# Optimization experiments

Hardware: AMD Instinct MI355X
Metric: run time of the kernel (lower is better)

## Reference

```python
import math
import jax, jax.numpy as jnp
import numpy as np

B, H, Nt, Nl, E = 4, 16, 512, 512, 64
P = H * E  # 1024, pre-projection embedding dim


def setup_inputs() -> dict:
    key = jax.random.key(0)
    ks = jax.random.split(key, 8)
    return {
        "projected_u": jax.random.normal(ks[0], (B, H, Nt, P), jnp.float32),
        "projected_b": jax.random.normal(ks[1], (B, H, Nt, 1), jnp.float32),
        "mu": jax.random.normal(ks[2], (B, Nl, P), jnp.float32),
        "logvar": jax.random.normal(ks[3], (B, Nl, P), jnp.float32) * 0.5,
        "pi": jax.random.uniform(ks[4], (B, Nl, 1), jnp.float32, 1e-3, 1.0),
        "w_v": jax.random.normal(ks[5], (H, E, P), jnp.float32) * 0.02,
        "b_v": jax.random.normal(ks[6], (H, E, Nl), jnp.float32) * 0.02,
        "attn_mask": jnp.zeros((B * H, 1, Nl), dtype=bool),  # True = masked
    }


def reference(projected_u, projected_b, mu, logvar, pi, w_v, b_v, attn_mask):
    Bq, Hq, Ntq, Pq = projected_u.shape
    Nlq = mu.shape[1]
    Eq = w_v.shape[1]
    prior_var_u = math.sqrt(Eq)

    var = jnp.exp(logvar)                         # [B,Nl,P]
    biased_var = var + prior_var_u                # [B,Nl,P]

    # float additive mask [B*H,1,Nl]: -inf where attn_mask True or pi<=0
    pi_rep = jnp.repeat(pi, Hq, axis=0)           # [B*H,Nl,1]
    am = jnp.where(attn_mask, -jnp.inf, 0.0)
    am = am + jnp.where(pi_rep.transpose(0, 2, 1) <= 0, -jnp.inf, 0.0)
    masked = jnp.isneginf(am).transpose(0, 2, 1)  # [B*H,Nl,1]

    # scores [B,H,Nt,Nl]
    attn = jnp.einsum('bhmp,bnp->bhmn', projected_u, mu / biased_var) + projected_b

    pi_c = jnp.maximum(pi_rep, jnp.finfo(pi_rep.dtype).tiny)
    t1 = jnp.where(masked, 0.0, jnp.log(pi_c))                                  # [B*H,Nl,1]
    t2 = 0.5 * jnp.sum((mu / jnp.sqrt(biased_var)) ** 2, axis=-1, keepdims=True)  # [B,Nl,1]
    t2 = jnp.repeat(t2, Hq, axis=0)                                             # [B*H,Nl,1]
    t3 = jnp.where(masked, 0.0, jnp.log(jnp.repeat(biased_var, Hq, axis=0)))    # [B*H,Nl,P]
    t3 = jnp.sum(0.5 * t3, axis=-1, keepdims=True)                              # [B*H,Nl,1]

    attn = attn + (t1 - t2 - t3).reshape(Bq, Hq, Nlq, 1).transpose(0, 1, 3, 2)  # [B,H,1,Nl]
    attn = attn + am.reshape(Bq, Hq, 1, Nlq)
    attn = jax.nn.softmax(attn, axis=-1)                                        # [B,H,Nt,Nl]

    # denoised values: interpolation between query projection and means
    out = (jnp.einsum('bhmn,bnp->bhmp', attn, var / biased_var) * projected_u
           + jnp.einsum('bhmn,bnp->bhmp', attn, (prior_var_u / biased_var) * mu))  # [B,H,Nt,P]
    out = (jnp.einsum('bhmp,hep->bhme', out, w_v)
           + jnp.einsum('bhmn,hen->bhme', attn, b_v))                              # [B,H,Nt,E]
    return (out.reshape(Bq * Hq, Ntq, Eq), attn.reshape(Bq * Hq, Ntq, Nlq))
```

## Files before the change

### kernel.cpp

```cpp
#include <hip/hip_runtime.h>
#include <cstdint>
#include <cstddef>
#include <cmath>

#define B_  4
#define H_  16
#define NT  512
#define NL  512
#define E_  64
#define P_  1024
#define HE  1024
#define BH  64

typedef __attribute__((ext_vector_type(8))) short short8;
typedef __attribute__((ext_vector_type(4))) float f32x4;
typedef unsigned short u16;

#define MFMA(a, b, c) __builtin_amdgcn_mfma_f32_16x16x32_bf16(a, b, c, 0, 0, 0)

static __device__ inline u16 f2bf_rne(float f) {
  unsigned u = __float_as_uint(f);
  unsigned r = u + 0x7FFFu + ((u >> 16) & 1u);
  return (u16)(r >> 16);
}

static __device__ inline void gl_lds16(const void* g, void* l) {
  __builtin_amdgcn_global_load_lds(
      (const __attribute__((address_space(1))) void*)g,
      (__attribute__((address_space(3))) void*)l, 16, 0, 0);
}

__global__ __launch_bounds__(256) void k_precompute(
    const float* __restrict__ mu, const float* __restrict__ logvar,
    const float* __restrict__ pi, u16* __restrict__ mobv_hi,
    u16* __restrict__ mobv_lo, u16* __restrict__ ibvT,
    float* __restrict__ bias) {
  const int bn = blockIdx.x;
  const int b = bn >> 9, n = bn & 511;
  const int t = threadIdx.x;
  const size_t base = (size_t)bn * P_;
  float t2 = 0.f, t3 = 0.f;
#pragma unroll
  for (int i = 0; i < P_ / 256; ++i) {
    const int p = t + i * 256;
    const float lv  = logvar[base + p];
    const float v   = expf(lv);
    const float bv  = v + 8.0f;
    const float inv = 1.0f / bv;
    const float m   = mu[base + p];
    const float x   = m * inv;
    const unsigned bits = __float_as_uint(x);
    mobv_hi[base + p] = (u16)(bits >> 16);
    const float r = x - __uint_as_float(bits & 0xFFFF0000u);
    mobv_lo[base + p] = (u16)(__float_as_uint(r) >> 16);
    ibvT[((size_t)b * P_ + p) * NL + n] = f2bf_rne(inv);
    t2 += m * x;
    t3 += logf(bv);
  }
  __shared__ float r2[256];
  __shared__ float r3[256];
  r2[t] = t2; r3[t] = t3;
  __syncthreads();
  for (int s = 128; s > 0; s >>= 1) {
    if (t < s) { r2[t] += r2[t + s]; r3[t] += r3[t + s]; }
    __syncthreads();
  }
  if (t == 0) {
    const float pv = pi[bn];
    float bb;
    if (pv <= 0.f) bb = -INFINITY;
    else bb = logf(fmaxf(pv, 1.17549435e-38f)) - 0.5f * r2[0] - 0.5f * r3[0];
    bias[bn] = bb;
  }
}

__global__ __launch_bounds__(256) void k_wvcast(const float* __restrict__ wv,
                                                u16* __restrict__ wvb) {
  const int i = (blockIdx.x * 256 + threadIdx.x) * 4;
  const float4 f = *(const float4*)&wv[i];
  wvb[i + 0] = f2bf_rne(f.x);
  wvb[i + 1] = f2bf_rne(f.y);
  wvb[i + 2] = f2bf_rne(f.z);
  wvb[i + 3] = f2bf_rne(f.w);
}

__global__ __launch_bounds__(256) void k_w2p(
    const u16* __restrict__ mobv_hi, const u16* __restrict__ mobv_lo,
    const u16* __restrict__ wvb, const float* __restrict__ bv_,
    u16* __restrict__ W2pT) {
  const int b    = blockIdx.z;
  const int row0 = blockIdx.x * 64;
  const int col0 = blockIdx.y * 128;
  const int t = threadIdx.x;
  const int wave = t >> 6, lane = t & 63;
  const int l16 = lane & 15, sel = lane >> 4;
  const int mrow = (wave >> 1) * 32, ncol = (wave & 1) * 64;

  __shared__ u16 Ah[64 * 32];
  __shared__ u16 Al[64 * 32];
  __shared__ u16 Bs[128 * 32];

  const u16* Abh = mobv_hi + ((size_t)b * NL + row0) * P_;
  const u16* Abl = mobv_lo + ((size_t)b * NL + row0) * P_;
  const u16* Bb  = wvb + (size_t)col0 * P_;

  f32x4 acc[2][4];
#pragma unroll
  for (int i = 0; i < 2; ++i)
#pragma unroll
    for (int j = 0; j < 4; ++j) acc[i][j] = (f32x4){0.f, 0.f, 0.f, 0.f};

  for (int k0 = 0; k0 < P_; k0 += 32) {
    {
      const int c = t;
      const int row = c >> 2, k8 = (c & 3) ^ ((row >> 1) & 3);
      gl_lds16(Abh + (size_t)row * P_ + k0 + k8 * 8, &Ah[wave * 64 * 8]);
      gl_lds16(Abl + (size_t)row * P_ + k0 + k8 * 8, &Al[wave * 64 * 8]);
    }
#pragma unroll
    for (int i = 0; i < 2; ++i) {
      const int c = t + i * 256;
      const int row = c >> 2, k8 = (c & 3) ^ ((row >> 1) & 3);
      gl_lds16(Bb + (size_t)row * P_ + k0 + k8 * 8,
               &Bs[(i * 256 + wave * 64) * 8]);
    }
    __syncthreads();
    short8 ah[2], al[2], bf[4];
#pragma unroll
    for (int mt = 0; mt < 2; ++mt) {
      const int r = mrow + mt * 16 + l16;
      const int ch = sel ^ ((r >> 1) & 3);
      ah[mt] = *(const short8*)&Ah[r * 32 + ch * 8];
      al[mt] = *(const short8*)&Al[r * 32 + ch * 8];
    }
#pragma unroll
    for (int nt = 0; nt < 4; ++nt) {
      const int r = ncol + nt * 16 + l16;
      const int ch = sel ^ ((r >> 1) & 3);
      bf[nt] = *(const short8*)&Bs[r * 32 + ch * 8];
    }
#pragma unroll
    for (int mt = 0; mt < 2; ++mt)
#pragma unroll
      for (int nt = 0; nt < 4; ++nt) {
        acc[mt][nt] = MFMA(ah[mt], bf[nt], acc[mt][nt]);
        acc[mt][nt] = MFMA(al[mt], bf[nt], acc[mt][nt]);
      }
    __syncthreads();
  }
#pragma unroll
  for (int mt = 0; mt < 2; ++mt) {
    const int nbase = row0 + mrow + mt * 16 + sel * 4;
#pragma unroll
    for (int nt = 0; nt < 4; ++nt) {
      const int he = col0 + ncol + nt * 16 + l16;
      const float4 bvv = *(const float4*)&bv_[(size_t)he * NL + nbase];
      ushort4 o;
      o.x = f2bf_rne(8.0f * acc[mt][nt][0] + bvv.x);
      o.y = f2bf_rne(8.0f * acc[mt][nt][1] + bvv.y);
      o.z = f2bf_rne(8.0f * acc[mt][nt][2] + bvv.z);
      o.w = f2bf_rne(8.0f * acc[mt][nt][3] + bvv.w);
      *(ushort4*)&W2pT[((size_t)b * HE + he) * NL + nbase] = o;
    }
  }
}

__global__ __launch_bounds__(256) void k_scores(
    const float* __restrict__ U, const u16* __restrict__ mobv_hi,
    const u16* __restrict__ mobv_lo, const float* __restrict__ pb,
    const float* __restrict__ bias, const uint8_t* __restrict__ mask,
    float* __restrict__ attn) {
  const int b    = blockIdx.z;
  const int row0 = blockIdx.x * 128;
  const int col0 = blockIdx.y * 128;
  const int t = threadIdx.x;
  const int wave = t >> 6, lane = t & 63;
  const int l16 = lane & 15, sel = lane >> 4;
  const int mrow = (wave >> 1) * 64, ncol = (wave & 1) * 64;

  __shared__ u16 Ah[128 * 32];
  __shared__ u16 Al[128 * 32];
  __shared__ u16 Bh[128 * 32];
  __shared__ u16 Bl[128 * 32];

  const u16* Bbh = mobv_hi + ((size_t)b * NL + col0) * P_;
  const u16* Bbl = mobv_lo + ((size_t)b * NL + col0) * P_;

  const int arow = t >> 1;
  const int ak   = (t & 1) * 16;
  const float* Aptr = U + ((size_t)b * 8192 + row0 + arow) * P_ + ak;
  const int asw = (arow >> 1) & 3;
  const int ch0 = ((t & 1) * 2 + 0) ^ asw;
  const int ch1 = ((t & 1) * 2 + 1) ^ asw;
  u16* AhW0 = &Ah[arow * 32 + ch0 * 8];
  u16* AhW1 = &Ah[arow * 32 + ch1 * 8];
  u16* AlW0 = &Al[arow * 32 + ch0 * 8];
  u16* AlW1 = &Al[arow * 32 + ch1 * 8];

  f32x4 acc[4][4];
#pragma unroll
  for (int i = 0; i < 4; ++i)
#pragma unroll
    for (int j = 0; j < 4; ++j) acc[i][j] = (f32x4){0.f, 0.f, 0.f, 0.f};

  for (int k0 = 0; k0 < P_; k0 += 32) {
    const float4 a0 = *(const float4*)&Aptr[k0 + 0];
    const float4 a1 = *(const float4*)&Aptr[k0 + 4];
    const float4 a2 = *(const float4*)&Aptr[k0 + 8];
    const float4 a3 = *(const float4*)&Aptr[k0 + 12];
#pragma unroll
    for (int i = 0; i < 2; ++i) {
      const int c = t + i * 256;
      const int row = c >> 2, k8 = (c & 3) ^ ((row >> 1) & 3);
      gl_lds16(Bbh + (size_t)row * P_ + k0 + k8 * 8,
               &Bh[(i * 256 + wave * 64) * 8]);
      gl_lds16(Bbl + (size_t)row * P_ + k0 + k8 * 8,
               &Bl[(i * 256 + wave * 64) * 8]);
    }
    const float av[16] = {a0.x, a0.y, a0.z, a0.w, a1.x, a1.y, a1.z, a1.w,
                          a2.x, a2.y, a2.z, a2.w, a3.x, a3.y, a3.z, a3.w};
    short8 h0, h1, l0, l1;
#pragma unroll
    for (int j = 0; j < 8; ++j) {
      unsigned bits = __float_as_uint(av[j]);
      h0[j] = (short)(bits >> 16);
      float rr = av[j] - __uint_as_float(bits & 0xFFFF0000u);
      l0[j] = (short)(__float_as_uint(rr) >> 16);
      bits = __float_as_uint(av[8 + j]);
      h1[j] = (short)(bits >> 16);
      rr = av[8 + j] - __uint_as_float(bits & 0xFFFF0000u);
      l1[j] = (short)(__float_as_uint(rr) >> 16);
    }
    *(short8*)AhW0 = h0;
    *(short8*)AhW1 = h1;
    *(short8*)AlW0 = l0;
    *(short8*)AlW1 = l1;
    __syncthreads();

    short8 ah[4], al[4], bh[4], bl[4];
#pragma unroll
    for (int mt = 0; mt < 4; ++mt) {
      const int r = mrow + mt * 16 + l16;
      const int ch = sel ^ ((r >> 1) & 3);
      ah[mt] = *(const short8*)&Ah[r * 32 + ch * 8];
      al[mt] = *(const short8*)&Al[r * 32 + ch * 8];
    }
#pragma unroll
    for (int nt = 0; nt < 4; ++nt) {
      const int r = ncol + nt * 16 + l16;
      const int ch = sel ^ ((r >> 1) & 3);
      bh[nt] = *(const short8*)&Bh[r * 32 + ch * 8];
      bl[nt] = *(const short8*)&Bl[r * 32 + ch * 8];
    }
#pragma unroll
    for (int mt = 0; mt < 4; ++mt)
#pragma unroll
      for (int nt = 0; nt < 4; ++nt) {
        acc[mt][nt] = MFMA(ah[mt], bh[nt], acc[mt][nt]);
        acc[mt][nt] = MFMA(ah[mt], bl[nt], acc[mt][nt]);
        acc[mt][nt] = MFMA(al[mt], bh[nt], acc[mt][nt]);
      }
    __syncthreads();
  }

  const int bh_ = b * H_ + (row0 >> 9);
  float pbv[4][4];
#pragma unroll
  for (int mt = 0; mt < 4; ++mt)
#pragma unroll
    for (int r = 0; r < 4; ++r)
      pbv[mt][r] = pb[(size_t)b * 8192 + row0 + mrow + mt * 16 + sel * 4 + r];
#pragma unroll
  for (int nt = 0; nt < 4; ++nt) {
    const int n = col0 + ncol + nt * 16 + l16;
    const float bcol = bias[b * NL + n];
    const bool mk = mask[(size_t)bh_ * NL + n] != 0;
#pragma unroll
    for (int mt = 0; mt < 4; ++mt) {
#pragma unroll
      for (int r = 0; r < 4; ++r) {
        const int row = row0 + mrow + mt * 16 + sel * 4 + r;
        float s = acc[mt][nt][r] + pbv[mt][r] + bcol;
        if (mk) s = -INFINITY;
        attn[((size_t)b * 8192 + row) * NL + n] = s;
      }
    }
  }
}

__global__ __launch_bounds__(256) void k_softmax(float* __restrict__ attn,
                                                 u16* __restrict__ attn_bf) {
  const int t = threadIdx.x;
  const int wave = t >> 6, lane = t & 63;
  const size_t r = (size_t)blockIdx.x * 4 + wave;
  float* row = attn + r * NL;
  const float4 v0 = ((const float4*)row)[lane * 2];
  const float4 v1 = ((const float4*)row)[lane * 2 + 1];
  float m = fmaxf(fmaxf(fmaxf(v0.x, v0.y), fmaxf(v0.z, v0.w)),
                  fmaxf(fmaxf(v1.x, v1.y), fmaxf(v1.z, v1.w)));
#pragma unroll
  for (int off = 32; off > 0; off >>= 1) m = fmaxf(m, __shfl_xor(m, off, 64));
  float e[8];
  e[0] = expf(v0.x - m); e[1] = expf(v0.y - m);
  e[2] = expf(v0.z - m); e[3] = expf(v0.w - m);
  e[4] = expf(v1.x - m); e[5] = expf(v1.y - m);
  e[6] = expf(v1.z - m); e[7] = expf(v1.w - m);
  float s = ((e[0] + e[1]) + (e[2] + e[3])) + ((e[4] + e[5]) + (e[6] + e[7]));
#pragma unroll
  for (int off = 32; off > 0; off >>= 1) s += __shfl_xor(s, off, 64);
  const float inv = 1.0f / s;
  float4 o0, o1;
  o0.x = e[0] * inv; o0.y = e[1] * inv; o0.z = e[2] * inv; o0.w = e[3] * inv;
  o1.x = e[4] * inv; o1.y = e[5] * inv; o1.z = e[6] * inv; o1.w = e[7] * inv;
  ((float4*)row)[lane * 2] = o0;
  ((float4*)row)[lane * 2 + 1] = o1;
  ushort4 b0, b1;
  b0.x = f2bf_rne(o0.x); b0.y = f2bf_rne(o0.y);
  b0.z = f2bf_rne(o0.z); b0.w = f2bf_rne(o0.w);
  b1.x = f2bf_rne(o1.x); b1.y = f2bf_rne(o1.y);
  b1.z = f2bf_rne(o1.z); b1.w = f2bf_rne(o1.w);
  ((ushort4*)(attn_bf + r * NL))[lane * 2] = b0;
  ((ushort4*)(attn_bf + r * NL))[lane * 2 + 1] = b1;
}

__global__ __launch_bounds__(256) void k_mid(
    const u16* __restrict__ attn_bf, const u16* __restrict__ ibvT,
    const float* __restrict__ U, u16* __restrict__ opS) {
  const int b    = blockIdx.z;
  const int row0 = blockIdx.x * 128;
  const int col0 = blockIdx.y * 128;
  const int t = threadIdx.x;
  const int wave = t >> 6, lane = t & 63;
  const int l16 = lane & 15, sel = lane >> 4;
  const int mrow = (wave >> 1) * 64, ncol = (wave & 1) * 64;

  __shared__ u16 As[128 * 32];
  __shared__ u16 Bs[128 * 32];

  const u16* Ab = attn_bf + ((size_t)b * 8192 + row0) * NL;
  const u16* Bb = ibvT + ((size_t)b * P_ + col0) * NL;

  f32x4 acc[4][4];
#pragma unroll
  for (int i = 0; i < 4; ++i)
#pragma unroll
    for (int j = 0; j < 4; ++j) acc[i][j] = (f32x4){0.f, 0.f, 0.f, 0.f};

  for (int k0 = 0; k0 < NL; k0 += 32) {
#pragma unroll
    for (int i = 0; i < 2; ++i) {
      const int c = t + i * 256;
      const int row = c >> 2, k8 = (c & 3) ^ ((row >> 1) & 3);
      gl_lds16(Ab + (size_t)row * NL + k0 + k8 * 8,
               &As[(i * 256 + wave * 64) * 8]);
      gl_lds16(Bb + (size_t)row * NL + k0 + k8 * 8,
               &Bs[(i * 256 + wave * 64) * 8]);
    }
    __syncthreads();
    short8 af[4], bf[4];
#pragma unroll
    for (int mt = 0; mt < 4; ++mt) {
      const int r = mrow + mt * 16 + l16;
      const int ch = sel ^ ((r >> 1) & 3);
      af[mt] = *(const short8*)&As[r * 32 + ch * 8];
    }
#pragma unroll
    for (int nt = 0; nt < 4; ++nt) {
      const int r = ncol + nt * 16 + l16;
      const int ch = sel ^ ((r >> 1) & 3);
      bf[nt] = *(const short8*)&Bs[r * 32 + ch * 8];
    }
#pragma unroll
    for (int mt = 0; mt < 4; ++mt)
#pragma unroll
      for (int nt = 0; nt < 4; ++nt)
        acc[mt][nt] = MFMA(af[mt], bf[nt], acc[mt][nt]);
    __syncthreads();
  }

#pragma unroll
  for (int mt = 0; mt < 4; ++mt) {
#pragma unroll
    for (int r = 0; r < 4; ++r) {
      const int m = row0 + mrow + mt * 16 + sel * 4 + r;
      const float* Urow = U + ((size_t)b * 8192 + m) * P_;
      u16* orow = opS + ((size_t)b * 8192 + m) * P_;
#pragma unroll
      for (int nt = 0; nt < 4; ++nt) {
        const int p = col0 + ncol + nt * 16 + l16;
        const float u = Urow[p];
        orow[p] = f2bf_rne((1.0f - 8.0f * acc[mt][nt][r]) * u);
      }
    }
  }
}

__global__ __launch_bounds__(256) void k_out2(
    const u16* __restrict__ opS, const u16* __restrict__ attn_bf,
    const u16* __restrict__ wvb, const u16* __restrict__ W2pT,
    float* __restrict__ out) {
  const int bh = blockIdx.y;
  const int b = bh >> 4, h = bh & 15;
  const int row0g = bh * NT + blockIdx.x * 64;
  const int t = threadIdx.x;
  const int wave = t >> 6, lane = t & 63;
  const int l16 = lane & 15, sel = lane >> 4;
  const int mrow = (wave >> 1) * 32, ncol = (wave & 1) * 32;

  __shared__ u16 As[64 * 64];
  __shared__ u16 Bs[64 * 64];

  f32x4 acc[2][2];
#pragma unroll
  for (int i = 0; i < 2; ++i)
#pragma unroll
    for (int j = 0; j < 2; ++j) acc[i][j] = (f32x4){0.f, 0.f, 0.f, 0.f};

  const u16* Ab1 = opS + (size_t)row0g * P_;
  const u16* Bb1 = wvb + (size_t)(h * 64) * P_;
  for (int k0 = 0; k0 < P_; k0 += 64) {
#pragma unroll
    for (int i = 0; i < 2; ++i) {
      const int c = t + i * 256;
      const int row = c >> 3, k8 = (c & 7) ^ (row & 7);
      gl_lds16(Ab1 + (size_t)row * P_ + k0 + k8 * 8,
               &As[(i * 256 + wave * 64) * 8]);
      gl_lds16(Bb1 + (size_t)row * P_ + k0 + k8 * 8,
               &Bs[(i * 256 + wave * 64) * 8]);
    }
    __syncthreads();
    short8 af[2][2], bf[2][2];
#pragma unroll
    for (int mt = 0; mt < 2; ++mt) {
      const int r = mrow + mt * 16 + l16;
#pragma unroll
      for (int kk = 0; kk < 2; ++kk) {
        const int ch = (kk * 4 + sel) ^ (r & 7);
        af[mt][kk] = *(const short8*)&As[r * 64 + ch * 8];
      }
    }
#pragma unroll
    for (int nt = 0; nt < 2; ++nt) {
      const int r = ncol + nt * 16 + l16;
#pragma unroll
      for (int kk = 0; kk < 2; ++kk) {
        const int ch = (kk * 4 + sel) ^ (r & 7);
        bf[nt][kk] = *(const short8*)&Bs[r * 64 + ch * 8];
      }
    }
#pragma unroll
    for (int mt = 0; mt < 2; ++mt)
#pragma unroll
      for (int nt = 0; nt < 2; ++nt) {
        acc[mt][nt] = MFMA(af[mt][0], bf[nt][0], acc[mt][nt]);
        acc[mt][nt] = MFMA(af[mt][1], bf[nt][1], acc[mt][nt]);
      }
    __syncthreads();
  }

  const u16* Ab2 = attn_bf + (size_t)row0g * NL;
  const u16* Bb2 = W2pT + ((size_t)b * HE + h * 64) * NL;
  for (int k0 = 0; k0 < NL; k0 += 64) {
#pragma unroll
    for (int i = 0; i < 2; ++i) {
      const int c = t + i * 256;
      const int row = c >> 3, k8 = (c & 7) ^ (row & 7);
      gl_lds16(Ab2 + (size_t)row * NL + k0 + k8 * 8,
               &As[(i * 256 + wave * 64) * 8]);
      gl_lds16(Bb2 + (size_t)row * NL + k0 + k8 * 8,
               &Bs[(i * 256 + wave * 64) * 8]);
    }
    __syncthreads();
    short8 af[2][2], bf[2][2];
#pragma unroll
    for (int mt = 0; mt < 2; ++mt) {
      const int r = mrow + mt * 16 + l16;
#pragma unroll
      for (int kk = 0; kk < 2; ++kk) {
        const int ch = (kk * 4 + sel) ^ (r & 7);
        af[mt][kk] = *(const short8*)&As[r * 64 + ch * 8];
      }
    }
#pragma unroll
    for (int nt = 0; nt < 2; ++nt) {
      const int r = ncol + nt * 16 + l16;
#pragma unroll
      for (int kk = 0; kk < 2; ++kk) {
        const int ch = (kk * 4 + sel) ^ (r & 7);
        bf[nt][kk] = *(const short8*)&Bs[r * 64 + ch * 8];
      }
    }
#pragma unroll
    for (int mt = 0; mt < 2; ++mt)
#pragma unroll
      for (int nt = 0; nt < 2; ++nt) {
        acc[mt][nt] = MFMA(af[mt][0], bf[nt][0], acc[mt][nt]);
        acc[mt][nt] = MFMA(af[mt][1], bf[nt][1], acc[mt][nt]);
      }
    __syncthreads();
  }

#pragma unroll
  for (int mt = 0; mt < 2; ++mt)
#pragma unroll
    for (int nt = 0; nt < 2; ++nt)
#pragma unroll
      for (int r = 0; r < 4; ++r) {
        const int row = row0g + mrow + mt * 16 + sel * 4 + r;
        const int e = ncol + nt * 16 + l16;
        out[(size_t)row * E_ + e] = acc[mt][nt][r];
      }
}

extern "C" void kernel_launch(void* const* d_in, const int* in_sizes, int n_in,
                              void* d_out, int out_size, void* d_ws, size_t ws_size,
                              hipStream_t stream) {
  const float*   u    = (const float*)d_in[0];
  const float*   pb   = (const float*)d_in[1];
  const float*   mu   = (const float*)d_in[2];
  const float*   logv = (const float*)d_in[3];
  const float*   pi   = (const float*)d_in[4];
  const float*   wv   = (const float*)d_in[5];
  const float*   bv   = (const float*)d_in[6];
  const uint8_t* mask = (const uint8_t*)d_in[7];

  float* out  = (float*)d_out;
  float* attn = out + (size_t)BH * NT * E_;

  u16*   mobv_hi = (u16*)d_ws;
  u16*   mobv_lo = mobv_hi + (size_t)B_ * NL * P_;
  u16*   ibvT    = mobv_lo + (size_t)B_ * NL * P_;
  u16*   W2pT    = ibvT + (size_t)B_ * P_ * NL;
  u16*   wvb     = W2pT + (size_t)B_ * HE * NL;
  float* bias    = (float*)(wvb + (size_t)HE * P_);
  u16*   attn_bf = (u16*)(bias + (size_t)B_ * NL);
  u16*   opS     = attn_bf + (size_t)BH * NT * NL;

  k_precompute<<<B_ * NL, 256, 0, stream>>>(mu, logv, pi, mobv_hi, mobv_lo,
                                            ibvT, bias);
  k_wvcast<<<(HE * P_) / 1024, 256, 0, stream>>>(wv, wvb);
  k_w2p<<<dim3(NL / 64, HE / 128, B_), 256, 0, stream>>>(mobv_hi, mobv_lo, wvb,
                                                         bv, W2pT);
  k_scores<<<dim3(8192 / 128, NL / 128, B_), 256, 0, stream>>>(
      u, mobv_hi, mobv_lo, pb, bias, mask, attn);
  k_softmax<<<(B_ * H_ * NT) / 4, 256, 0, stream>>>(attn, attn_bf);
  k_mid<<<dim3(8192 / 128, P_ / 128, B_), 256, 0, stream>>>(attn_bf, ibvT, u,
                                                            opS);
  k_out2<<<dim3(NT / 64, BH), 256, 0, stream>>>(opS, attn_bf, wvb, W2pT, out);
}
```

Measured before the change: 489.1 us.

## Double-buffer LDS tiles in score and mid GEMMs, stage fp32 A via direct loads

```diff
diff --git a/kernel.cpp b/kernel.cpp
--- a/kernel.cpp
+++ b/kernel.cpp
@@ -178,24 +178,13 @@
   const int l16 = lane & 15, sel = lane >> 4;
   const int mrow = (wave >> 1) * 64, ncol = (wave & 1) * 64;
 
-  __shared__ u16 Ah[128 * 32];
-  __shared__ u16 Al[128 * 32];
-  __shared__ u16 Bh[128 * 32];
-  __shared__ u16 Bl[128 * 32];
-
-  const u16* Bbh = mobv_hi + ((size_t)b * NL + col0) * P_;
-  const u16* Bbl = mobv_lo + ((size_t)b * NL + col0) * P_;
-
-  const int arow = t >> 1;
-  const int ak   = (t & 1) * 16;
-  const float* Aptr = U + ((size_t)b * 8192 + row0 + arow) * P_ + ak;
-  const int asw = (arow >> 1) & 3;
-  const int ch0 = ((t & 1) * 2 + 0) ^ asw;
-  const int ch1 = ((t & 1) * 2 + 1) ^ asw;
-  u16* AhW0 = &Ah[arow * 32 + ch0 * 8];
-  u16* AhW1 = &Ah[arow * 32 + ch1 * 8];
-  u16* AlW0 = &Al[arow * 32 + ch0 * 8];
-  u16* AlW1 = &Al[arow * 32 + ch1 * 8];
+  __shared__ float Af[2][128 * 32];
+  __shared__ u16   Bh[2][128 * 32];
+  __shared__ u16   Bl[2][128 * 32];
+
+  const float* Ab  = U + ((size_t)b * 8192 + row0) * P_;
+  const u16*   Bbh = mobv_hi + ((size_t)b * NL + col0) * P_;
+  const u16*   Bbl = mobv_lo + ((size_t)b * NL + col0) * P_;
 
   f32x4 acc[4][4];
 #pragma unroll
@@ -203,54 +192,54 @@
 #pragma unroll
     for (int j = 0; j < 4; ++j) acc[i][j] = (f32x4){0.f, 0.f, 0.f, 0.f};
 
-  for (int k0 = 0; k0 < P_; k0 += 32) {
-    const float4 a0 = *(const float4*)&Aptr[k0 + 0];
-    const float4 a1 = *(const float4*)&Aptr[k0 + 4];
-    const float4 a2 = *(const float4*)&Aptr[k0 + 8];
-    const float4 a3 = *(const float4*)&Aptr[k0 + 12];
+  auto stage = [&](int buf, int k0) {
+#pragma unroll
+    for (int i = 0; i < 4; ++i) {
+      const int c = t + i * 256;
+      const int row = c >> 3, k4 = (c & 7) ^ (row & 7);
+      gl_lds16(Ab + (size_t)row * P_ + k0 + k4 * 4,
+               &Af[buf][(i * 256 + wave * 64) * 4]);
+    }
 #pragma unroll
     for (int i = 0; i < 2; ++i) {
       const int c = t + i * 256;
       const int row = c >> 2, k8 = (c & 3) ^ ((row >> 1) & 3);
       gl_lds16(Bbh + (size_t)row * P_ + k0 + k8 * 8,
-               &Bh[(i * 256 + wave * 64) * 8]);
+               &Bh[buf][(i * 256 + wave * 64) * 8]);
       gl_lds16(Bbl + (size_t)row * P_ + k0 + k8 * 8,
-               &Bl[(i * 256 + wave * 64) * 8]);
-    }
-    const float av[16] = {a0.x, a0.y, a0.z, a0.w, a1.x, a1.y, a1.z, a1.w,
-                          a2.x, a2.y, a2.z, a2.w, a3.x, a3.y, a3.z, a3.w};
-    short8 h0, h1, l0, l1;
-#pragma unroll
-    for (int j = 0; j < 8; ++j) {
-      unsigned bits = __float_as_uint(av[j]);
-      h0[j] = (short)(bits >> 16);
-      float rr = av[j] - __uint_as_float(bits & 0xFFFF0000u);
-      l0[j] = (short)(__float_as_uint(rr) >> 16);
-      bits = __float_as_uint(av[8 + j]);
-      h1[j] = (short)(bits >> 16);
-      rr = av[8 + j] - __uint_as_float(bits & 0xFFFF0000u);
-      l1[j] = (short)(__float_as_uint(rr) >> 16);
-    }
-    *(short8*)AhW0 = h0;
-    *(short8*)AhW1 = h1;
-    *(short8*)AlW0 = l0;
-    *(short8*)AlW1 = l1;
-    __syncthreads();
+               &Bl[buf][(i * 256 + wave * 64) * 8]);
+    }
+  };
+
+  stage(0, 0);
+  __syncthreads();
+  int cur = 0;
+  for (int k0 = 0; k0 < P_; k0 += 32) {
+    if (k0 + 32 < P_) stage(cur ^ 1, k0 + 32);
 
     short8 ah[4], al[4], bh[4], bl[4];
 #pragma unroll
     for (int mt = 0; mt < 4; ++mt) {
       const int r = mrow + mt * 16 + l16;
-      const int ch = sel ^ ((r >> 1) & 3);
-      ah[mt] = *(const short8*)&Ah[r * 32 + ch * 8];
-      al[mt] = *(const short8*)&Al[r * 32 + ch * 8];
+      const int c0 = (sel * 2) ^ (r & 7);
+      const int c1 = (sel * 2 + 1) ^ (r & 7);
+      const float4 f0 = *(const float4*)&Af[cur][r * 32 + c0 * 4];
+      const float4 f1 = *(const float4*)&Af[cur][r * 32 + c1 * 4];
+      const float fv[8] = {f0.x, f0.y, f0.z, f0.w, f1.x, f1.y, f1.z, f1.w};
+#pragma unroll
+      for (int j = 0; j < 8; ++j) {
+        const unsigned bits = __float_as_uint(fv[j]);
+        ah[mt][j] = (short)(bits >> 16);
+        const float rr = fv[j] - __uint_as_float(bits & 0xFFFF0000u);
+        al[mt][j] = (short)(__float_as_uint(rr) >> 16);
+      }
     }
 #pragma unroll
     for (int nt = 0; nt < 4; ++nt) {
       const int r = ncol + nt * 16 + l16;
       const int ch = sel ^ ((r >> 1) & 3);
-      bh[nt] = *(const short8*)&Bh[r * 32 + ch * 8];
-      bl[nt] = *(const short8*)&Bl[r * 32 + ch * 8];
+      bh[nt] = *(const short8*)&Bh[cur][r * 32 + ch * 8];
+      bl[nt] = *(const short8*)&Bl[cur][r * 32 + ch * 8];
     }
 #pragma unroll
     for (int mt = 0; mt < 4; ++mt)
@@ -261,6 +250,7 @@
         acc[mt][nt] = MFMA(al[mt], bh[nt], acc[mt][nt]);
       }
     __syncthreads();
+    cur ^= 1;
   }
 
   const int bh_ = b * H_ + (row0 >> 9);
@@ -334,8 +324,8 @@
   const int l16 = lane & 15, sel = lane >> 4;
   const int mrow = (wave >> 1) * 64, ncol = (wave & 1) * 64;
 
-  __shared__ u16 As[128 * 32];
-  __shared__ u16 Bs[128 * 32];
+  __shared__ u16 As[2][128 * 32];
+  __shared__ u16 Bs[2][128 * 32];
 
   const u16* Ab = attn_bf + ((size_t)b * 8192 + row0) * NL;
   const u16* Bb = ibvT + ((size_t)b * P_ + col0) * NL;
@@ -346,29 +336,35 @@
 #pragma unroll
     for (int j = 0; j < 4; ++j) acc[i][j] = (f32x4){0.f, 0.f, 0.f, 0.f};
 
-  for (int k0 = 0; k0 < NL; k0 += 32) {
+  auto stage = [&](int buf, int k0) {
 #pragma unroll
     for (int i = 0; i < 2; ++i) {
       const int c = t + i * 256;
       const int row = c >> 2, k8 = (c & 3) ^ ((row >> 1) & 3);
       gl_lds16(Ab + (size_t)row * NL + k0 + k8 * 8,
-               &As[(i * 256 + wave * 64) * 8]);
+               &As[buf][(i * 256 + wave * 64) * 8]);
       gl_lds16(Bb + (size_t)row * NL + k0 + k8 * 8,
-               &Bs[(i * 256 + wave * 64) * 8]);
-    }
-    __syncthreads();
+               &Bs[buf][(i * 256 + wave * 64) * 8]);
+    }
+  };
+
+  stage(0, 0);
+  __syncthreads();
+  int cur = 0;
+  for (int k0 = 0; k0 < NL; k0 += 32) {
+    if (k0 + 32 < NL) stage(cur ^ 1, k0 + 32);
     short8 af[4], bf[4];
 #pragma unroll
     for (int mt = 0; mt < 4; ++mt) {
       const int r = mrow + mt * 16 + l16;
       const int ch = sel ^ ((r >> 1) & 3);
-      af[mt] = *(const short8*)&As[r * 32 + ch * 8];
+      af[mt] = *(const short8*)&As[cur][r * 32 + ch * 8];
     }
 #pragma unroll
     for (int nt = 0; nt < 4; ++nt) {
       const int r = ncol + nt * 16 + l16;
       const int ch = sel ^ ((r >> 1) & 3);
-      bf[nt] = *(const short8*)&Bs[r * 32 + ch * 8];
+      bf[nt] = *(const short8*)&Bs[cur][r * 32 + ch * 8];
     }
 #pragma unroll
     for (int mt = 0; mt < 4; ++mt)
@@ -376,6 +372,7 @@
       for (int nt = 0; nt < 4; ++nt)
         acc[mt][nt] = MFMA(af[mt], bf[nt], acc[mt][nt]);
     __syncthreads();
+    cur ^= 1;
   }
 
 #pragma unroll
```

Result: slower. 510.0 us (+4.3%).
